# Kernel optimization log

Hardware: AMD Instinct MI355X
Metric: run time of the kernel (lower is better)

Reference implementation:

```python
import jax, jax.numpy as jnp
import numpy as np

N = 50000
E = 400000
C_IN = 32
H = 64
RATIO = 0.5
SEQ_LEN = 5


def setup_inputs() -> dict:
    key = jax.random.key(0)
    ks = jax.random.split(key, 12)
    x = jax.random.normal(ks[0], (N, C_IN), jnp.float32)
    row = jax.random.randint(ks[1], (E,), 0, N, jnp.int32)
    off = jax.random.randint(ks[2], (E,), 1, N, jnp.int32)
    col = ((row + off) % N).astype(jnp.int32)  # no self-loops
    edge_index = jnp.stack([row, col])
    mask = jax.random.uniform(ks[3], (N,)) < 0.5

    def g(k, shape, fan):
        return jax.random.normal(k, shape, jnp.float32) / np.float32(np.sqrt(fan))

    return {
        "x": x, "edge_index": edge_index, "mask": mask,
        "conv0_w": g(ks[4], (C_IN, H), C_IN), "conv0_b": jnp.zeros((H,), jnp.float32),
        "conv1_w": g(ks[5], (H, H), H), "conv1_b": jnp.zeros((H,), jnp.float32),
        "pool_w": g(ks[6], (H,), H),
        "up_w": g(ks[7], (H, H), H), "up_b": jnp.zeros((H,), jnp.float32),
        "lstm0_w_ih": g(ks[8], (4 * H, H), H), "lstm0_w_hh": g(ks[9], (4 * H, H), H),
        "lstm0_b_ih": jnp.zeros((4 * H,), jnp.float32), "lstm0_b_hh": jnp.zeros((4 * H,), jnp.float32),
        "fin_w_ih": g(ks[10], (4 * H, H), H), "fin_w_hh": g(ks[11], (4 * H, H), H),
        "fin_b_ih": jnp.zeros((4 * H,), jnp.float32), "fin_b_hh": jnp.zeros((4 * H,), jnp.float32),
    }


def _coalesce(row, col, w, n):
    # sum duplicate (row, col) entries; output sorted by (row, col)
    key = row.astype(np.int64) * n + col.astype(np.int64)
    uk, inv = np.unique(key, return_inverse=True)
    w2 = np.bincount(inv, weights=w.astype(np.float64), minlength=uk.shape[0]).astype(np.float32)
    return uk // n, uk % n, w2


def _augment_adj(row, col, w, n):
    # remove self loops, add self loops (weight 1), compute A @ A (sparse), remove self loops
    m = row != col
    row = np.concatenate([row[m].astype(np.int64), np.arange(n, dtype=np.int64)])
    col = np.concatenate([col[m].astype(np.int64), np.arange(n, dtype=np.int64)])
    w = np.concatenate([w[m].astype(np.float32), np.ones(n, np.float32)])
    row, col, w = _coalesce(row, col, w, n)  # CSR-ordered
    cnt = np.bincount(row, minlength=n)
    indptr = np.concatenate([[0], np.cumsum(cnt)])
    dk = cnt[col]                      # out-degree of middle node k for each edge (i,k)
    starts = indptr[col]
    total = int(dk.sum())
    seg = np.repeat(np.cumsum(dk) - dk, dk)
    gi = np.repeat(starts, dk) + (np.arange(total) - seg)
    oi = np.repeat(row, dk)
    oj = col[gi]
    ow = np.repeat(w, dk) * w[gi]
    r2, c2, w2 = _coalesce(oi, oj, ow, n)
    m2 = r2 != c2
    return r2[m2], c2[m2], w2[m2]


def _gcn(x, row, col, ew, n, W, b):
    # GCNConv(improved=True): self-loop weight 2.0, symmetric deg^-1/2 normalization,
    # aggregate messages at target (col)
    h = x @ W
    loop = jnp.arange(n, dtype=row.dtype)
    r = jnp.concatenate([row, loop])
    c = jnp.concatenate([col, loop])
    w = jnp.concatenate([ew, jnp.full((n,), 2.0, ew.dtype)])
    deg = jax.ops.segment_sum(w, c, num_segments=n)
    dinv = jnp.where(deg > 0, jax.lax.rsqrt(deg), 0.0)
    norm = dinv[r] * w * dinv[c]
    out = jax.ops.segment_sum(norm[:, None] * h[r], c, num_segments=n)
    return out + b


def _sequences(x, mi):
    # sliding window [idx-L+1, idx] per masked node, zero left-padded
    t = mi[:, None] + jnp.arange(SEQ_LEN)[None, :] - (SEQ_LEN - 1)  # [M, L]
    return jnp.where((t >= 0)[:, :, None], x[jnp.clip(t, 0)], 0.0)


def _lstm_last(seq, w_ih, w_hh, b_ih, b_hh):
    # torch LSTM gate order: i, f, g, o; zero init state; return last hidden
    h = jnp.zeros((seq.shape[0], w_hh.shape[1]), seq.dtype)
    c = jnp.zeros_like(h)
    def step(carry, xt):
        h, c = carry
        g = xt @ w_ih.T + h @ w_hh.T + b_ih + b_hh
        i, f, gg, o = jnp.split(g, 4, axis=-1)
        c = jax.nn.sigmoid(f) * c + jax.nn.sigmoid(i) * jnp.tanh(gg)
        h = jax.nn.sigmoid(o) * jnp.tanh(c)
        return (h, c), None
    (h, _), _ = jax.lax.scan(step, (h, c), jnp.swapaxes(seq, 0, 1))
    return h


def reference(x, edge_index, mask, conv0_w, conv0_b, conv1_w, conv1_b, pool_w,
              up_w, up_b, lstm0_w_ih, lstm0_w_hh, lstm0_b_ih, lstm0_b_hh,
              fin_w_ih, fin_w_hh, fin_b_ih, fin_b_hh):
    n = x.shape[0]
    row0, col0 = edge_index[0], edge_index[1]
    ew0 = jnp.ones((row0.shape[0],), x.dtype)

    # down conv 0
    x1 = jax.nn.relu(_gcn(x, row0, col0, ew0, n, conv0_w, conv0_b))

    # augment_adj: sparse (A+I)^2 without diagonal (structural, constant)
    r2, c2, w2 = _augment_adj(np.asarray(row0), np.asarray(col0),
                              np.ones(row0.shape[0], np.float32), n)

    # TopKPooling: score = tanh((x.w)/||w||), keep top ceil(ratio*n)
    score = jnp.tanh((x1 @ pool_w) / jnp.linalg.norm(pool_w))
    k = int(np.ceil(RATIO * n))
    perm = np.argsort(-np.asarray(score), kind="stable")[:k]
    remap = np.full(n, -1, np.int64)
    remap[perm] = np.arange(k)
    keep = (remap[r2] >= 0) & (remap[c2] >= 0)
    pr = jnp.asarray(remap[r2[keep]].astype(np.int32))
    pc = jnp.asarray(remap[c2[keep]].astype(np.int32))
    pw = jnp.asarray(w2[keep])
    permj = jnp.asarray(perm.astype(np.int32))
    xp = x1[permj] * score[permj][:, None]

    # down conv 1 on pooled graph
    x2 = jax.nn.relu(_gcn(xp, pr, pc, pw, k, conv1_w, conv1_b))

    # up path (depth=1): LSTM over skip features at masked nodes
    mi = jnp.asarray(np.where(np.asarray(mask))[0].astype(np.int32))
    h0 = _lstm_last(_sequences(x1, mi), lstm0_w_ih, lstm0_w_hh, lstm0_b_ih, lstm0_b_hh)
    res = x1.at[mi].set(h0)
    up = jnp.zeros_like(x1).at[permj].set(x2)
    xo = _gcn(res + up, row0, col0, ew0, n, up_w, up_b)  # last level: no activation

    # final LSTM on masked nodes
    hf = _lstm_last(_sequences(xo, mi), fin_w_ih, fin_w_hh, fin_b_ih, fin_b_hh)
    return xo.at[mi].set(hf)
```

## Files before the change

### kernel.cpp

```cpp
#include <hip/hip_runtime.h>
#include <math.h>

#define NN 50000
#define EE 400000
#define CINV 32
#define KKEEP 25000
#define SEQL 5
#define HASH_BITS 20
#define HASH_SIZE (1u<<HASH_BITS)
#define HASH_MASK (HASH_SIZE-1u)
#define HEMPTY 0xFFFFFFFFu
#define PSB 196

typedef float vf4 __attribute__((ext_vector_type(4)));

__device__ __forceinline__ float sigm(float x){ return __builtin_amdgcn_rcpf(1.f+__expf(-x)); }
__device__ __forceinline__ float ftanh(float x){ return 1.f - 2.f*__builtin_amdgcn_rcpf(1.f+__expf(2.f*x)); }

__global__ void k_init(uint2* __restrict__ hash, unsigned* __restrict__ hist,
                       int* __restrict__ degcnt, int* __restrict__ diagint,
                       int* __restrict__ fillc, int* __restrict__ minv,
                       unsigned* scal, unsigned long long* selp,
                       const float* __restrict__ w0, const float* __restrict__ b0i,
                       const float* __restrict__ b0h, const float* __restrict__ wf,
                       const float* __restrict__ bfi, const float* __restrict__ bfh,
                       float* __restrict__ WT0, float* __restrict__ WTf,
                       float* __restrict__ bs0, float* __restrict__ bsf){
  int i = blockIdx.x*256 + threadIdx.x;
  if (i < (int)HASH_SIZE) hash[i] = make_uint2(HEMPTY, 0u);
  if (i < 4*65536) hist[i] = 0u;
  if (i < NN){ degcnt[i]=0; diagint[i]=0; fillc[i]=0; minv[i]=-1; }
  if (i < 256*64){
    int g = i>>6, k = i&63;
    WT0[k*256+g] = w0[i];
    WTf[k*256+g] = wf[i];
  }
  if (i < 256){ bs0[i]=b0i[i]+b0h[i]; bsf[i]=bfi[i]+bfh[i]; }
  if (i == 0){ scal[0]=0u; scal[1]=0u; scal[3]=KKEEP; selp[0]=0ull; }
}

__global__ void k_phase2(const int* __restrict__ row, const int* __restrict__ col,
                         const int* __restrict__ mp, int* __restrict__ degcnt,
                         uint2* __restrict__ tab, unsigned* scal){
  int e = blockIdx.x*256 + threadIdx.x;
  if (e < EE){
    int c = col[e];
    atomicAdd(&degcnt[c], 1);
    unsigned key = (unsigned)row[e]*50000u + (unsigned)c;
    unsigned h = (key*2654435761u) >> (32-HASH_BITS);
    for(;;){
      unsigned old = atomicCAS(&tab[h].x, HEMPTY, key);
      if (old==HEMPTY || old==key){ atomicAdd(&tab[h].y, 1u); break; }
      h = (h+1)&HASH_MASK;
    }
  }
  if (e < NN/4){ if ((unsigned)mp[e] > 1u) atomicOr(&scal[1], 1u); }
}

__global__ void k_psum1(const int* __restrict__ deg, int* __restrict__ part,
                        int* __restrict__ bsum, float* __restrict__ dinv){
  __shared__ int sc[256];
  int b = blockIdx.x, t = threadIdx.x, i = b*256+t;
  int v = (i<NN) ? deg[i] : 0;
  if (i < NN) dinv[i] = rsqrtf((float)v + 2.0f);
  sc[t] = v; __syncthreads();
  for (int o=1;o<256;o<<=1){
    int x = (t>=o) ? sc[t-o] : 0;
    __syncthreads();
    sc[t] += x;
    __syncthreads();
  }
  if (i < NN) part[i] = sc[t]-v;
  if (t == 255) bsum[b] = sc[255];
}
__global__ void k_psum2(const int* __restrict__ bsum, int* __restrict__ boff){
  __shared__ int sc[256];
  int t = threadIdx.x;
  int v = (t<PSB) ? bsum[t] : 0;
  sc[t] = v; __syncthreads();
  for (int o=1;o<256;o<<=1){
    int x = (t>=o) ? sc[t-o] : 0;
    __syncthreads();
    sc[t] += x;
    __syncthreads();
  }
  if (t < PSB) boff[t] = sc[t]-v;
}
__global__ void k_psum3(const int* __restrict__ part, const int* __restrict__ boff,
                        int* __restrict__ indptr){
  int i = blockIdx.x*256 + threadIdx.x;
  if (i < NN) indptr[i] = part[i] + boff[blockIdx.x];
  if (i == 0) indptr[NN] = EE;
}

__global__ void k_phase4(const int* __restrict__ row, const int* __restrict__ col,
                         const int* __restrict__ indptr, int* __restrict__ fillc,
                         int* __restrict__ csr_r, const uint2* __restrict__ tab,
                         int* __restrict__ diagint, const void* __restrict__ mp,
                         unsigned* scal, int* __restrict__ mlist, int* __restrict__ minv){
  int idx = blockIdx.x*256 + threadIdx.x;
  if (idx < EE){
    int r = row[idx], c = col[idx];
    int pos = indptr[c] + atomicAdd(&fillc[c], 1);
    csr_r[pos] = r;
    unsigned rkey = (unsigned)c*50000u + (unsigned)r;
    unsigned h = (rkey*2654435761u) >> (32-HASH_BITS);
    for(;;){
      unsigned kk = tab[h].x;
      if (kk==rkey){ atomicAdd(&diagint[r], (int)tab[h].y); break; }
      if (kk==HEMPTY) break;
      h = (h+1)&HASH_MASK;
    }
  } else {
    int i = idx - EE;
    if (i < NN){
      int mv = scal[1] ? (int)((const unsigned char*)mp)[i] : ((const int*)mp)[i];
      if (mv){ int p = (int)atomicAdd(&scal[0], 1u); mlist[p] = i; minv[i] = p; }
    }
  }
}

__global__ void k_mm_h0v(const float* __restrict__ X, const float* __restrict__ W, float* __restrict__ Y){
  int idx = blockIdx.x*256 + threadIdx.x;
  if (idx >= NN*16) return;
  int i = idx>>4, fq = idx&15;
  const vf4* X4 = (const vf4*)&X[i*CINV];
  const vf4* W4 = (const vf4*)W;
  vf4 acc = {0.f,0.f,0.f,0.f};
  #pragma unroll
  for (int kq=0;kq<CINV/4;kq++){
    vf4 xv = X4[kq];
    #pragma unroll
    for (int u=0;u<4;u++) acc += xv[u] * W4[(kq*4+u)*16+fq];
  }
  ((vf4*)Y)[i*16+fq] = acc;
}
__global__ void k_mm64v(const float* __restrict__ X, const float* __restrict__ W, float* __restrict__ Y){
  int idx = blockIdx.x*256 + threadIdx.x;
  if (idx >= NN*16) return;
  int i = idx>>4, fq = idx&15;
  const vf4* X4 = (const vf4*)&X[i*64];
  const vf4* W4 = (const vf4*)W;
  vf4 acc = {0.f,0.f,0.f,0.f};
  #pragma unroll
  for (int kq=0;kq<16;kq++){
    vf4 xv = X4[kq];
    #pragma unroll
    for (int u=0;u<4;u++) acc += xv[u] * W4[(kq*4+u)*16+fq];
  }
  ((vf4*)Y)[i*16+fq] = acc;
}
__global__ void k_mm64sv(const float* __restrict__ X, const float* __restrict__ W,
                         const float* __restrict__ sc, const int* __restrict__ kp,
                         float* __restrict__ Y){
  int idx = blockIdx.x*256 + threadIdx.x;
  if (idx >= NN*16) return;
  int i = idx>>4, fq = idx&15;
  if (!kp[i]) return;
  const vf4* X4 = (const vf4*)&X[i*64];
  const vf4* W4 = (const vf4*)W;
  vf4 acc = {0.f,0.f,0.f,0.f};
  #pragma unroll
  for (int kq=0;kq<16;kq++){
    vf4 xv = X4[kq];
    #pragma unroll
    for (int u=0;u<4;u++) acc += xv[u] * W4[(kq*4+u)*16+fq];
  }
  float s = sc[i];
  acc *= s;
  ((vf4*)Y)[i*16+fq] = acc;
}

__global__ void g_gcn0(const int* __restrict__ indptr, const int* __restrict__ csr_r,
                       const float* __restrict__ dinv, const float* __restrict__ H,
                       const float* __restrict__ b, const float* __restrict__ pw,
                       float* __restrict__ out, unsigned long long* __restrict__ keys,
                       float* __restrict__ score, unsigned* __restrict__ hist){
  int node = blockIdx.x*4 + (threadIdx.x>>6), lane = threadIdx.x&63;
  if (node >= NN) return;
  int s = __builtin_amdgcn_readfirstlane(indptr[node]);
  int e = __builtin_amdgcn_readfirstlane(indptr[node+1]);
  int deg = e - s;
  float a0=0.f,a1=0.f,a2=0.f,a3=0.f;
  for (int base=0; base<deg; base+=64){
    int take = min(64, deg-base);
    bool act = lane < take;
    int ii = act ? csr_r[s+base+lane] : 0;
    float dv = act ? dinv[ii] : 0.f;
    int j=0;
    for (; j+4<=take; j+=4){
      int r0=__shfl(ii,j,64), r1=__shfl(ii,j+1,64), r2=__shfl(ii,j+2,64), r3=__shfl(ii,j+3,64);
      float d0=__shfl(dv,j,64), d1=__shfl(dv,j+1,64), d2=__shfl(dv,j+2,64), d3=__shfl(dv,j+3,64);
      a0 += d0*H[(size_t)r0*64+lane];
      a1 += d1*H[(size_t)r1*64+lane];
      a2 += d2*H[(size_t)r2*64+lane];
      a3 += d3*H[(size_t)r3*64+lane];
    }
    for (; j<take; j++){
      int r0=__shfl(ii,j,64); float d0=__shfl(dv,j,64);
      a0 += d0*H[(size_t)r0*64+lane];
    }
  }
  float acc = (a0+a1)+(a2+a3);
  float di = dinv[node];
  float v = di*acc + 2.f*di*di*H[(size_t)node*64+lane] + b[lane];
  float x1v = fmaxf(v, 0.f);
  out[(size_t)node*64+lane] = x1v;
  float pv = pw[lane];
  float nq = pv*pv;
  float dq = x1v*pv;
  for (int o=32;o;o>>=1){ nq += __shfl_down(nq, o, 64); dq += __shfl_down(dq, o, 64); }
  if (lane==0){
    float sv = tanhf(dq / sqrtf(nq));
    sv = sv + 0.0f;
    score[node] = sv;
    unsigned u = __float_as_uint(sv);
    unsigned asc = (u>>31) ? ~u : (u | 0x80000000u);
    unsigned desc = ~asc;
    keys[node] = (((unsigned long long)desc)<<32) | (unsigned)node;
    atomicAdd(&hist[desc>>16], 1u);
  }
}
__global__ void g_t2(const int* __restrict__ indptr, const int* __restrict__ csr_r,
                     const float* __restrict__ dinv1, const float* __restrict__ hp,
                     float* __restrict__ t2){
  int node = blockIdx.x*4 + (threadIdx.x>>6), lane = threadIdx.x&63;
  if (node >= NN) return;
  int s = __builtin_amdgcn_readfirstlane(indptr[node]);
  int e = __builtin_amdgcn_readfirstlane(indptr[node+1]);
  int deg = e - s;
  float a0 = dinv1[node]*hp[(size_t)node*64+lane];
  float a1 = 0.f;
  for (int base=0; base<deg; base+=64){
    int take = min(64, deg-base);
    bool act = lane < take;
    int ii = act ? csr_r[s+base+lane] : 0;
    float dv = act ? dinv1[ii] : 0.f;
    int j=0;
    for (; j+2<=take; j+=2){
      float d0=__shfl(dv,j,64), d1=__shfl(dv,j+1,64);
      int r0=__shfl(ii,j,64), r1=__shfl(ii,j+1,64);
      if (d0!=0.f) a0 += d0*hp[(size_t)r0*64+lane];
      if (d1!=0.f) a1 += d1*hp[(size_t)r1*64+lane];
    }
    for (; j<take; j++){
      float d0=__shfl(dv,j,64); int r0=__shfl(ii,j,64);
      if (d0!=0.f) a0 += d0*hp[(size_t)r0*64+lane];
    }
  }
  t2[(size_t)node*64+lane] = a0+a1;
}
__global__ void g_agg2y(const int* __restrict__ indptr, const int* __restrict__ csr_r,
                        const float* __restrict__ t2, const float* __restrict__ hp,
                        const float* __restrict__ dinv1, const int* __restrict__ diagint,
                        const int* __restrict__ kp, const float* __restrict__ b1,
                        const float* __restrict__ C, const float* __restrict__ Hbuf,
                        const int* __restrict__ minv, float* __restrict__ D){
  int node = blockIdx.x*4 + (threadIdx.x>>6), lane = threadIdx.x&63;
  if (node >= NN) return;
  int mv = minv[node];
  float base = (mv >= 0) ? Hbuf[(size_t)mv*64+lane] : C[(size_t)node*64+lane];
  float add = 0.f;
  if (kp[node]){
    int s = __builtin_amdgcn_readfirstlane(indptr[node]);
    int e = __builtin_amdgcn_readfirstlane(indptr[node+1]);
    int deg = e - s;
    float a0 = t2[(size_t)node*64+lane];
    float a1=0.f,a2=0.f,a3=0.f;
    for (int bs2=0; bs2<deg; bs2+=64){
      int take = min(64, deg-bs2);
      bool act = lane < take;
      int ii = act ? csr_r[s+bs2+lane] : 0;
      int j=0;
      for (; j+4<=take; j+=4){
        int r0=__shfl(ii,j,64), r1=__shfl(ii,j+1,64), r2=__shfl(ii,j+2,64), r3=__shfl(ii,j+3,64);
        a0 += t2[(size_t)r0*64+lane];
        a1 += t2[(size_t)r1*64+lane];
        a2 += t2[(size_t)r2*64+lane];
        a3 += t2[(size_t)r3*64+lane];
      }
      for (; j<take; j++){
        int r0=__shfl(ii,j,64);
        a0 += t2[(size_t)r0*64+lane];
      }
    }
    float acc = (a0+a1)+(a2+a3);
    float di = dinv1[node], hv = hp[(size_t)node*64+lane];
    float diag = (float)(diagint[node] + 1);
    float v = di*(acc - diag*di*hv) + 2.f*di*di*hv + b1[lane];
    add = fmaxf(v, 0.f);
  }
  D[(size_t)node*64+lane] = base + add;
}
__global__ void g_up(const int* __restrict__ indptr, const int* __restrict__ csr_r,
                     const float* __restrict__ dinv, const float* __restrict__ H,
                     const float* __restrict__ b, float* __restrict__ xo, float* __restrict__ out){
  int node = blockIdx.x*4 + (threadIdx.x>>6), lane = threadIdx.x&63;
  if (node >= NN) return;
  int s = __builtin_amdgcn_readfirstlane(indptr[node]);
  int e = __builtin_amdgcn_readfirstlane(indptr[node+1]);
  int deg = e - s;
  float a0=0.f,a1=0.f,a2=0.f,a3=0.f;
  for (int base=0; base<deg; base+=64){
    int take = min(64, deg-base);
    bool act = lane < take;
    int ii = act ? csr_r[s+base+lane] : 0;
    float dv = act ? dinv[ii] : 0.f;
    int j=0;
    for (; j+4<=take; j+=4){
      int r0=__shfl(ii,j,64), r1=__shfl(ii,j+1,64), r2=__shfl(ii,j+2,64), r3=__shfl(ii,j+3,64);
      float d0=__shfl(dv,j,64), d1=__shfl(dv,j+1,64), d2=__shfl(dv,j+2,64), d3=__shfl(dv,j+3,64);
      a0 += d0*H[(size_t)r0*64+lane];
      a1 += d1*H[(size_t)r1*64+lane];
      a2 += d2*H[(size_t)r2*64+lane];
      a3 += d3*H[(size_t)r3*64+lane];
    }
    for (; j<take; j++){
      int r0=__shfl(ii,j,64); float d0=__shfl(dv,j,64);
      a0 += d0*H[(size_t)r0*64+lane];
    }
  }
  float acc = (a0+a1)+(a2+a3);
  float di = dinv[node];
  float v = di*acc + 2.f*di*di*H[(size_t)node*64+lane] + b[lane];
  xo[(size_t)node*64+lane] = v; out[(size_t)node*64+lane] = v;
}

__global__ void k_hist(const unsigned long long* __restrict__ keys, unsigned* __restrict__ hist,
                       const unsigned long long* __restrict__ selp, int round){
  int i = blockIdx.x*256 + threadIdx.x;
  if (i >= NN) return;
  unsigned long long key = keys[i];
  int shift = 48 - 16*round;
  if ((key>>(shift+16)) == selp[0])
    atomicAdd(&hist[(unsigned)((key>>shift)&0xFFFFull)], 1u);
}
__global__ void k_pick(const unsigned* __restrict__ hist, unsigned long long* selp, unsigned* scal){
  __shared__ unsigned csum[256];
  __shared__ unsigned bins[256];
  __shared__ int schunk;
  int t = threadIdx.x;
  const uint4* h4 = (const uint4*)(hist + t*256);
  unsigned s = 0;
  #pragma unroll 8
  for (int j=0;j<64;j++){ uint4 v = h4[j]; s += v.x+v.y+v.z+v.w; }
  csum[t] = s;
  __syncthreads();
  if (t==0){
    unsigned rem = scal[3];
    int chunk = 255;
    for (int c2=0;c2<256;c2++){ unsigned cc=csum[c2]; if (rem>cc) rem-=cc; else { chunk=c2; break; } }
    schunk = chunk; scal[3] = rem;
  }
  __syncthreads();
  bins[t] = hist[schunk*256 + t];
  __syncthreads();
  if (t==0){
    unsigned rem = scal[3];
    int bin = schunk*256 + 255;
    for (int b=0;b<256;b++){ unsigned hv=bins[b]; if (rem>hv) rem-=hv; else { bin = schunk*256 + b; break; } }
    selp[0] = (selp[0]<<16) | (unsigned long long)(unsigned)bin;
    scal[3] = rem;
  }
}
__global__ void k_tsg(const int* __restrict__ indptr, const int* __restrict__ csr_r,
                      const unsigned long long* __restrict__ keys,
                      const unsigned long long* __restrict__ selp,
                      int* __restrict__ kp, int* __restrict__ ts){
  int i = blockIdx.x*256 + threadIdx.x;
  if (i >= NN) return;
  unsigned long long sp = selp[0];
  int s = indptr[i], e = indptr[i+1];
  int self = (keys[i] <= sp) ? 1 : 0;
  kp[i] = self;
  int acc = self;
  for (int j=s;j<e;j++) acc += (keys[csr_r[j]] <= sp) ? 1 : 0;
  ts[i] = acc;
}
__global__ void k_csg(const int* __restrict__ indptr, const int* __restrict__ csr_r,
                      const int* __restrict__ ts, const int* __restrict__ diagint,
                      const int* __restrict__ kp, float* __restrict__ dinv1){
  int i = blockIdx.x*256 + threadIdx.x;
  if (i >= NN) return;
  int s = indptr[i], e = indptr[i+1];
  int acc = ts[i];
  for (int j=s;j<e;j++) acc += ts[csr_r[j]];
  dinv1[i] = kp[i] ? rsqrtf((float)(acc - diagint[i] - 1) + 2.0f) : 0.f;
}

__global__ __launch_bounds__(256) void k_xw(const float* __restrict__ src,
        const float* __restrict__ WT, const float* __restrict__ bsum,
        float* __restrict__ XW){
  __shared__ vf4 Wl[4096];
  int t = threadIdx.x;
  const vf4* Wg = (const vf4*)WT;
  for (int u=t; u<4096; u+=256) Wl[u] = Wg[u];
  int fq = t & 63, wv = t >> 6;
  vf4 bias = ((const vf4*)bsum)[fq];
  __syncthreads();
  for (int g = blockIdx.x*4 + wv; g < NN/4; g += gridDim.x*4){
    int n0 = g*4;
    const vf4* X4 = (const vf4*)&src[(size_t)n0*64];
    vf4 a0=bias, a1=bias, a2=bias, a3=bias;
    #pragma unroll 4
    for (int kq=0;kq<16;kq++){
      vf4 x0 = X4[kq], x1 = X4[16+kq], x2 = X4[32+kq], x3 = X4[48+kq];
      vf4 w0 = Wl[(kq*4+0)*64+fq];
      vf4 w1 = Wl[(kq*4+1)*64+fq];
      vf4 w2 = Wl[(kq*4+2)*64+fq];
      vf4 w3 = Wl[(kq*4+3)*64+fq];
      a0 += x0.x*w0 + x0.y*w1 + x0.z*w2 + x0.w*w3;
      a1 += x1.x*w0 + x1.y*w1 + x1.z*w2 + x1.w*w3;
      a2 += x2.x*w0 + x2.y*w1 + x2.z*w2 + x2.w*w3;
      a3 += x3.x*w0 + x3.y*w1 + x3.z*w2 + x3.w*w3;
    }
    vf4* Y = (vf4*)XW;
    Y[(size_t)n0*64 + fq]       = a0;
    Y[(size_t)n0*64 + 64 + fq]  = a1;
    Y[(size_t)n0*64 + 128 + fq] = a2;
    Y[(size_t)n0*64 + 192 + fq] = a3;
  }
}

__global__ __launch_bounds__(256) void k_rec(const float* __restrict__ XW,
        const float* __restrict__ whh, const float* __restrict__ bsum,
        const int* __restrict__ mlist, const unsigned* __restrict__ scal,
        float* __restrict__ dst, int scatter){
  int M = (int)scal[0];
  if (M < 0 || M > NN) M = 0;
  int w = threadIdx.x>>6, lane = threadIdx.x&63;
  int r = w*64 + lane;
  const vf4* g4 = (const vf4*)&whh[(size_t)r*64];
  vf4 wh[16];
  #pragma unroll
  for (int j=0;j<16;j++) wh[j] = g4[j];
  __shared__ float sh[8][64];
  __shared__ float gates[8][4][64];
  int ntask = (M+7)>>3;
  for (int task = blockIdx.x; task < ntask; task += gridDim.x){
    int m0 = task*8 + 2*w, m1 = m0+1;
    bool v0 = (m0 < M), v1 = (m1 < M);
    int n0 = mlist[v0 ? m0 : (M-1)];
    int n1 = mlist[v1 ? m1 : (M-1)];
    n0 = min(max(n0, 0), NN-1);
    n1 = min(max(n1, 0), NN-1);
    float c0, h0, c1, h1;
    float x0,x1,x2,x3, y0,y1,y2,y3;
    {
      int ra = n0 - (SEQL-1), rb = n1 - (SEQL-1);
      if (ra >= 0){
        const float* p = &XW[(size_t)ra*256];
        x0=p[lane]; x1=p[64+lane]; x2=p[128+lane]; x3=p[192+lane];
      } else { x0=bsum[lane]; x1=bsum[64+lane]; x2=bsum[128+lane]; x3=bsum[192+lane]; }
      if (rb >= 0){
        const float* p = &XW[(size_t)rb*256];
        y0=p[lane]; y1=p[64+lane]; y2=p[128+lane]; y3=p[192+lane];
      } else { y0=bsum[lane]; y1=bsum[64+lane]; y2=bsum[128+lane]; y3=bsum[192+lane]; }
      c0 = sigm(x0)*ftanh(x2); h0 = sigm(x3)*ftanh(c0);
      c1 = sigm(y0)*ftanh(y2); h1 = sigm(y3)*ftanh(c1);
      sh[2*w][lane] = h0;
      sh[2*w+1][lane] = h1;
    }
    __syncthreads();
    for (int t=1;t<SEQL;t++){
      int ra = n0 - (SEQL-1) + t, rb = n1 - (SEQL-1) + t;
      if (ra >= 0){
        const float* p = &XW[(size_t)ra*256];
        x0=p[lane]; x1=p[64+lane]; x2=p[128+lane]; x3=p[192+lane];
      } else { x0=bsum[lane]; x1=bsum[64+lane]; x2=bsum[128+lane]; x3=bsum[192+lane]; }
      if (rb >= 0){
        const float* p = &XW[(size_t)rb*256];
        y0=p[lane]; y1=p[64+lane]; y2=p[128+lane]; y3=p[192+lane];
      } else { y0=bsum[lane]; y1=bsum[64+lane]; y2=bsum[128+lane]; y3=bsum[192+lane]; }
      vf4 a0={0,0,0,0},a1={0,0,0,0},a2={0,0,0,0},a3={0,0,0,0};
      vf4 a4={0,0,0,0},a5={0,0,0,0},a6={0,0,0,0},a7={0,0,0,0};
      #pragma unroll
      for (int j=0;j<16;j++){
        vf4 wj = wh[j];
        a0 += (*(const vf4*)&sh[0][j*4]) * wj;
        a1 += (*(const vf4*)&sh[1][j*4]) * wj;
        a2 += (*(const vf4*)&sh[2][j*4]) * wj;
        a3 += (*(const vf4*)&sh[3][j*4]) * wj;
        a4 += (*(const vf4*)&sh[4][j*4]) * wj;
        a5 += (*(const vf4*)&sh[5][j*4]) * wj;
        a6 += (*(const vf4*)&sh[6][j*4]) * wj;
        a7 += (*(const vf4*)&sh[7][j*4]) * wj;
      }
      gates[0][w][lane] = a0.x+a0.y+a0.z+a0.w;
      gates[1][w][lane] = a1.x+a1.y+a1.z+a1.w;
      gates[2][w][lane] = a2.x+a2.y+a2.z+a2.w;
      gates[3][w][lane] = a3.x+a3.y+a3.z+a3.w;
      gates[4][w][lane] = a4.x+a4.y+a4.z+a4.w;
      gates[5][w][lane] = a5.x+a5.y+a5.z+a5.w;
      gates[6][w][lane] = a6.x+a6.y+a6.z+a6.w;
      gates[7][w][lane] = a7.x+a7.y+a7.z+a7.w;
      __syncthreads();
      int p0 = 2*w, p1 = 2*w+1;
      float gi = gates[p0][0][lane] + x0;
      float gf = gates[p0][1][lane] + x1;
      float gg = gates[p0][2][lane] + x2;
      float go = gates[p0][3][lane] + x3;
      c0 = sigm(gf)*c0 + sigm(gi)*ftanh(gg);
      h0 = sigm(go)*ftanh(c0);
      sh[p0][lane] = h0;
      gi = gates[p1][0][lane] + y0;
      gf = gates[p1][1][lane] + y1;
      gg = gates[p1][2][lane] + y2;
      go = gates[p1][3][lane] + y3;
      c1 = sigm(gf)*c1 + sigm(gi)*ftanh(gg);
      h1 = sigm(go)*ftanh(c1);
      sh[p1][lane] = h1;
      __syncthreads();
    }
    if (v0){
      size_t o = scatter ? ((size_t)n0*64 + lane) : ((size_t)m0*64 + lane);
      dst[o] = h0;
    }
    if (v1){
      size_t o = scatter ? ((size_t)n1*64 + lane) : ((size_t)m1*64 + lane);
      dst[o] = h1;
    }
  }
}

extern "C" void kernel_launch(void* const* d_in, const int* in_sizes, int n_in,
                              void* d_out, int out_size, void* d_ws, size_t ws_size,
                              hipStream_t stream) {
  const float* x   = (const float*)d_in[0];
  const int*   ei  = (const int*)d_in[1];
  const int*   row = ei;
  const int*   col = ei + EE;
  const void*  mp  = d_in[2];
  const float* W0  = (const float*)d_in[3];
  const float* b0  = (const float*)d_in[4];
  const float* W1  = (const float*)d_in[5];
  const float* b1  = (const float*)d_in[6];
  const float* pw  = (const float*)d_in[7];
  const float* Wu  = (const float*)d_in[8];
  const float* bu  = (const float*)d_in[9];
  const float* l0wih=(const float*)d_in[10];
  const float* l0whh=(const float*)d_in[11];
  const float* l0bih=(const float*)d_in[12];
  const float* l0bhh=(const float*)d_in[13];
  const float* lfwih=(const float*)d_in[14];
  const float* lfwhh=(const float*)d_in[15];
  const float* lfbih=(const float*)d_in[16];
  const float* lfbhh=(const float*)d_in[17];

  char* wp = (char*)d_ws;
  auto alloc = [&](size_t bytes)->char*{ char* p = wp; wp += ((bytes+255)/256)*256; return p; };
  float* A     = (float*)alloc((size_t)NN*64*4);
  float* B     = (float*)alloc((size_t)NN*64*4);
  float* C     = (float*)alloc((size_t)NN*64*4);
  float* D     = (float*)alloc((size_t)NN*64*4);
  float* Ebuf  = (float*)alloc((size_t)NN*64*4);
  float* Hbuf  = (float*)alloc((size_t)NN*64*4);
  float* XW    = (float*)alloc((size_t)NN*256*4);
  float* WT0   = (float*)alloc((size_t)256*64*4);
  float* WTf   = (float*)alloc((size_t)256*64*4);
  float* bs0   = (float*)alloc((size_t)256*4);
  float* bsf   = (float*)alloc((size_t)256*4);
  float* score = (float*)alloc((size_t)NN*4);
  float* dinv0 = (float*)alloc((size_t)NN*4);
  float* dinv1 = (float*)alloc((size_t)NN*4);
  unsigned long long* keys = (unsigned long long*)alloc((size_t)NN*8);
  int* degcnt  = (int*)alloc((size_t)NN*4);
  int* diagint = (int*)alloc((size_t)NN*4);
  int* ts      = (int*)alloc((size_t)NN*4);
  int* kp      = (int*)alloc((size_t)NN*4);
  int* mlist   = (int*)alloc((size_t)NN*4);
  int* minv    = (int*)alloc((size_t)NN*4);
  int* indptr  = (int*)alloc((size_t)(NN+1)*4);
  int* part    = (int*)alloc((size_t)NN*4);
  int* fillc   = (int*)alloc((size_t)NN*4);
  int* bsum    = (int*)alloc((size_t)256*4);
  int* boff    = (int*)alloc((size_t)256*4);
  int* csr_r   = (int*)alloc((size_t)EE*4);
  uint2* hash  = (uint2*)alloc((size_t)HASH_SIZE*8);
  unsigned* hist=(unsigned*)alloc((size_t)4*65536*4);
  unsigned* scal=(unsigned*)alloc(256);
  unsigned long long* selp = (unsigned long long*)(scal + 4);

  #define GRID1(n) dim3(((n)+255)/256), dim3(256), 0, stream
  #define GRIDW dim3((NN+3)/4), dim3(256), 0, stream

  k_init<<<GRID1(HASH_SIZE)>>>(hash, hist, degcnt, diagint, fillc, minv,
                               scal, selp, l0wih, l0bih, l0bhh, lfwih, lfbih, lfbhh,
                               WT0, WTf, bs0, bsf);
  k_phase2<<<GRID1(EE)>>>(row, col, (const int*)mp, degcnt, hash, scal);
  k_psum1<<<dim3(PSB),dim3(256),0,stream>>>(degcnt, part, bsum, dinv0);
  k_psum2<<<dim3(1),dim3(256),0,stream>>>(bsum, boff);
  k_psum3<<<dim3(PSB),dim3(256),0,stream>>>(part, boff, indptr);
  k_phase4<<<GRID1(EE+NN)>>>(row, col, indptr, fillc, csr_r, hash, diagint, mp, scal, mlist, minv);

  k_mm_h0v<<<GRID1(NN*16)>>>(x, W0, A);
  g_gcn0<<<GRIDW>>>(indptr, csr_r, dinv0, A, b0, pw, C, keys, score, hist);

  k_pick<<<dim3(1),dim3(256),0,stream>>>(hist, selp, scal);
  for (int r2=1;r2<4;r2++){
    k_hist<<<GRID1(NN)>>>(keys, hist + r2*65536, selp, r2);
    k_pick<<<dim3(1),dim3(256),0,stream>>>(hist + r2*65536, selp, scal);
  }
  k_tsg<<<GRID1(NN)>>>(indptr, csr_r, keys, selp, kp, ts);
  k_csg<<<GRID1(NN)>>>(indptr, csr_r, ts, diagint, kp, dinv1);

  k_mm64sv<<<GRID1(NN*16)>>>(C, W1, score, kp, Ebuf);
  g_t2<<<GRIDW>>>(indptr, csr_r, dinv1, Ebuf, A);

  k_xw<<<dim3(512),dim3(256),0,stream>>>(C, WT0, bs0, XW);
  k_rec<<<dim3(2048),dim3(256),0,stream>>>(XW, l0whh, bs0, mlist, scal, Hbuf, 0);

  g_agg2y<<<GRIDW>>>(indptr, csr_r, A, Ebuf, dinv1, diagint, kp, b1, C, Hbuf, minv, D);

  k_mm64v<<<GRID1(NN*16)>>>(D, Wu, Ebuf);
  g_up<<<GRIDW>>>(indptr, csr_r, dinv0, Ebuf, bu, B, (float*)d_out);

  k_xw<<<dim3(512),dim3(256),0,stream>>>(B, WTf, bsf, XW);
  k_rec<<<dim3(2048),dim3(256),0,stream>>>(XW, lfwhh, bsf, mlist, scal, (float*)d_out, 1);
  #undef GRIDW
  #undef GRID1
}
```

Before: 688.7 us.

## Fuse small kernels to cut launches and shrink LSTM tasks to one sequence per wave

Folds the first dense matmul into the edge hashing kernel and the pooled matmul into the degree-count kernel. It also merges the two prefix-sum passes so each block rescans the block sums itself, which removes three launches from a launch-bound pipeline. The LSTM recurrence kernel now handles one sequence per wave (four per block) instead of two, with fewer blocks launched. This cuts per-wave register and shared-memory work but halves the sequences sharing each loaded recurrent weight set.

```diff
diff --git a/kernel.cpp b/kernel.cpp
--- a/kernel.cpp
+++ b/kernel.cpp
@@ -41,12 +41,14 @@
 
 __global__ void k_phase2(const int* __restrict__ row, const int* __restrict__ col,
                          const int* __restrict__ mp, int* __restrict__ degcnt,
-                         uint2* __restrict__ tab, unsigned* scal){
-  int e = blockIdx.x*256 + threadIdx.x;
-  if (e < EE){
-    int c = col[e];
+                         uint2* __restrict__ tab, unsigned* scal,
+                         const float* __restrict__ X, const float* __restrict__ W,
+                         float* __restrict__ Y){
+  int idx = blockIdx.x*256 + threadIdx.x;
+  if (idx < EE){
+    int c = col[idx];
     atomicAdd(&degcnt[c], 1);
-    unsigned key = (unsigned)row[e]*50000u + (unsigned)c;
+    unsigned key = (unsigned)row[idx]*50000u + (unsigned)c;
     unsigned h = (key*2654435761u) >> (32-HASH_BITS);
     for(;;){
       unsigned old = atomicCAS(&tab[h].x, HEMPTY, key);
@@ -54,7 +56,20 @@
       h = (h+1)&HASH_MASK;
     }
   }
-  if (e < NN/4){ if ((unsigned)mp[e] > 1u) atomicOr(&scal[1], 1u); }
+  if (idx < NN/4){ if ((unsigned)mp[idx] > 1u) atomicOr(&scal[1], 1u); }
+  if (idx < NN*16){
+    int i = idx>>4, fq = idx&15;
+    const vf4* X4 = (const vf4*)&X[i*CINV];
+    const vf4* W4 = (const vf4*)W;
+    vf4 acc = {0.f,0.f,0.f,0.f};
+    #pragma unroll
+    for (int kq=0;kq<CINV/4;kq++){
+      vf4 xv = X4[kq];
+      #pragma unroll
+      for (int u=0;u<4;u++) acc += xv[u] * W4[(kq*4+u)*16+fq];
+    }
+    ((vf4*)Y)[i*16+fq] = acc;
+  }
 }
 
 __global__ void k_psum1(const int* __restrict__ deg, int* __restrict__ part,
@@ -73,7 +88,8 @@
   if (i < NN) part[i] = sc[t]-v;
   if (t == 255) bsum[b] = sc[255];
 }
-__global__ void k_psum2(const int* __restrict__ bsum, int* __restrict__ boff){
+__global__ void k_psum3(const int* __restrict__ part, const int* __restrict__ bsum,
+                        int* __restrict__ indptr){
   __shared__ int sc[256];
   int t = threadIdx.x;
   int v = (t<PSB) ? bsum[t] : 0;
@@ -84,12 +100,10 @@
     sc[t] += x;
     __syncthreads();
   }
-  if (t < PSB) boff[t] = sc[t]-v;
-}
-__global__ void k_psum3(const int* __restrict__ part, const int* __restrict__ boff,
-                        int* __restrict__ indptr){
-  int i = blockIdx.x*256 + threadIdx.x;
-  if (i < NN) indptr[i] = part[i] + boff[blockIdx.x];
+  int bb = blockIdx.x;
+  int ex = sc[bb] - ((bb<PSB) ? bsum[bb] : 0);
+  int i = bb*256 + t;
+  if (i < NN) indptr[i] = part[i] + ex;
   if (i == 0) indptr[NN] = EE;
 }
 
@@ -120,21 +134,6 @@
   }
 }
 
-__global__ void k_mm_h0v(const float* __restrict__ X, const float* __restrict__ W, float* __restrict__ Y){
-  int idx = blockIdx.x*256 + threadIdx.x;
-  if (idx >= NN*16) return;
-  int i = idx>>4, fq = idx&15;
-  const vf4* X4 = (const vf4*)&X[i*CINV];
-  const vf4* W4 = (const vf4*)W;
-  vf4 acc = {0.f,0.f,0.f,0.f};
-  #pragma unroll
-  for (int kq=0;kq<CINV/4;kq++){
-    vf4 xv = X4[kq];
-    #pragma unroll
-    for (int u=0;u<4;u++) acc += xv[u] * W4[(kq*4+u)*16+fq];
-  }
-  ((vf4*)Y)[i*16+fq] = acc;
-}
 __global__ void k_mm64v(const float* __restrict__ X, const float* __restrict__ W, float* __restrict__ Y){
   int idx = blockIdx.x*256 + threadIdx.x;
   if (idx >= NN*16) return;
@@ -148,26 +147,6 @@
     #pragma unroll
     for (int u=0;u<4;u++) acc += xv[u] * W4[(kq*4+u)*16+fq];
   }
-  ((vf4*)Y)[i*16+fq] = acc;
-}
-__global__ void k_mm64sv(const float* __restrict__ X, const float* __restrict__ W,
-                         const float* __restrict__ sc, const int* __restrict__ kp,
-                         float* __restrict__ Y){
-  int idx = blockIdx.x*256 + threadIdx.x;
-  if (idx >= NN*16) return;
-  int i = idx>>4, fq = idx&15;
-  if (!kp[i]) return;
-  const vf4* X4 = (const vf4*)&X[i*64];
-  const vf4* W4 = (const vf4*)W;
-  vf4 acc = {0.f,0.f,0.f,0.f};
-  #pragma unroll
-  for (int kq=0;kq<16;kq++){
-    vf4 xv = X4[kq];
-    #pragma unroll
-    for (int u=0;u<4;u++) acc += xv[u] * W4[(kq*4+u)*16+fq];
-  }
-  float s = sc[i];
-  acc *= s;
   ((vf4*)Y)[i*16+fq] = acc;
 }
 
@@ -377,15 +356,34 @@
   for (int j=s;j<e;j++) acc += (keys[csr_r[j]] <= sp) ? 1 : 0;
   ts[i] = acc;
 }
-__global__ void k_csg(const int* __restrict__ indptr, const int* __restrict__ csr_r,
-                      const int* __restrict__ ts, const int* __restrict__ diagint,
-                      const int* __restrict__ kp, float* __restrict__ dinv1){
-  int i = blockIdx.x*256 + threadIdx.x;
-  if (i >= NN) return;
-  int s = indptr[i], e = indptr[i+1];
-  int acc = ts[i];
-  for (int j=s;j<e;j++) acc += ts[csr_r[j]];
-  dinv1[i] = kp[i] ? rsqrtf((float)(acc - diagint[i] - 1) + 2.0f) : 0.f;
+__global__ void k_csgmm(const int* __restrict__ indptr, const int* __restrict__ csr_r,
+                        const int* __restrict__ ts, const int* __restrict__ diagint,
+                        const int* __restrict__ kp, float* __restrict__ dinv1,
+                        const float* __restrict__ X, const float* __restrict__ W,
+                        const float* __restrict__ sc, float* __restrict__ Y){
+  int idx = blockIdx.x*256 + threadIdx.x;
+  if (idx < NN*16){
+    int i = idx>>4, fq = idx&15;
+    if (!kp[i]) return;
+    const vf4* X4 = (const vf4*)&X[i*64];
+    const vf4* W4 = (const vf4*)W;
+    vf4 acc = {0.f,0.f,0.f,0.f};
+    #pragma unroll
+    for (int kq=0;kq<16;kq++){
+      vf4 xv = X4[kq];
+      #pragma unroll
+      for (int u=0;u<4;u++) acc += xv[u] * W4[(kq*4+u)*16+fq];
+    }
+    acc *= sc[i];
+    ((vf4*)Y)[i*16+fq] = acc;
+  } else {
+    int i = idx - NN*16;
+    if (i >= NN) return;
+    int s = indptr[i], e = indptr[i+1];
+    int acc = ts[i];
+    for (int j=s;j<e;j++) acc += ts[csr_r[j]];
+    dinv1[i] = kp[i] ? rsqrtf((float)(acc - diagint[i] - 1) + 2.0f) : 0.f;
+  }
 }
 
 __global__ __launch_bounds__(256) void k_xw(const float* __restrict__ src,
@@ -434,46 +432,38 @@
   vf4 wh[16];
   #pragma unroll
   for (int j=0;j<16;j++) wh[j] = g4[j];
-  __shared__ float sh[8][64];
-  __shared__ float gates[8][4][64];
-  int ntask = (M+7)>>3;
+  __shared__ float sh[4][64];
+  __shared__ float gates[4][4][64];
+  int ntask = (M+3)>>2;
   for (int task = blockIdx.x; task < ntask; task += gridDim.x){
-    int m0 = task*8 + 2*w, m1 = m0+1;
-    bool v0 = (m0 < M), v1 = (m1 < M);
-    int n0 = mlist[v0 ? m0 : (M-1)];
-    int n1 = mlist[v1 ? m1 : (M-1)];
-    n0 = min(max(n0, 0), NN-1);
-    n1 = min(max(n1, 0), NN-1);
-    float c0, h0, c1, h1;
-    float x0,x1,x2,x3, y0,y1,y2,y3;
+    int m = task*4 + w;
+    bool valid = (m < M);
+    int node = mlist[valid ? m : (M-1)];
+    node = min(max(node, 0), NN-1);
+    float c, h;
+    float x0,x1,x2,x3;
     {
-      int ra = n0 - (SEQL-1), rb = n1 - (SEQL-1);
-      if (ra >= 0){
-        const float* p = &XW[(size_t)ra*256];
+      int rowi = node - (SEQL-1);
+      if (rowi >= 0){
+        const float* p = &XW[(size_t)rowi*256];
         x0=p[lane]; x1=p[64+lane]; x2=p[128+lane]; x3=p[192+lane];
-      } else { x0=bsum[lane]; x1=bsum[64+lane]; x2=bsum[128+lane]; x3=bsum[192+lane]; }
-      if (rb >= 0){
-        const float* p = &XW[(size_t)rb*256];
-        y0=p[lane]; y1=p[64+lane]; y2=p[128+lane]; y3=p[192+lane];
-      } else { y0=bsum[lane]; y1=bsum[64+lane]; y2=bsum[128+lane]; y3=bsum[192+lane]; }
-      c0 = sigm(x0)*ftanh(x2); h0 = sigm(x3)*ftanh(c0);
-      c1 = sigm(y0)*ftanh(y2); h1 = sigm(y3)*ftanh(c1);
-      sh[2*w][lane] = h0;
-      sh[2*w+1][lane] = h1;
+      } else {
+        x0=bsum[lane]; x1=bsum[64+lane]; x2=bsum[128+lane]; x3=bsum[192+lane];
+      }
+      c = sigm(x0)*ftanh(x2);
+      h = sigm(x3)*ftanh(c);
+      sh[w][lane] = h;
     }
     __syncthreads();
     for (int t=1;t<SEQL;t++){
-      int ra = n0 - (SEQL-1) + t, rb = n1 - (SEQL-1) + t;
-      if (ra >= 0){
-        const float* p = &XW[(size_t)ra*256];
+      int rowi = node - (SEQL-1) + t;
+      if (rowi >= 0){
+        const float* p = &XW[(size_t)rowi*256];
         x0=p[lane]; x1=p[64+lane]; x2=p[128+lane]; x3=p[192+lane];
-      } else { x0=bsum[lane]; x1=bsum[64+lane]; x2=bsum[128+lane]; x3=bsum[192+lane]; }
-      if (rb >= 0){
-        const float* p = &XW[(size_t)rb*256];
-        y0=p[lane]; y1=p[64+lane]; y2=p[128+lane]; y3=p[192+lane];
-      } else { y0=bsum[lane]; y1=bsum[64+lane]; y2=bsum[128+lane]; y3=bsum[192+lane]; }
-      vf4 a0={0,0,0,0},a1={0,0,0,0},a2={0,0,0,0},a3={0,0,0,0};
-      vf4 a4={0,0,0,0},a5={0,0,0,0},a6={0,0,0,0},a7={0,0,0,0};
+      } else {
+        x0=bsum[lane]; x1=bsum[64+lane]; x2=bsum[128+lane]; x3=bsum[192+lane];
+      }
+      vf4 a0={0,0,0,0}, a1={0,0,0,0}, a2={0,0,0,0}, a3={0,0,0,0};
       #pragma unroll
       for (int j=0;j<16;j++){
         vf4 wj = wh[j];
@@ -481,44 +471,24 @@
         a1 += (*(const vf4*)&sh[1][j*4]) * wj;
         a2 += (*(const vf4*)&sh[2][j*4]) * wj;
         a3 += (*(const vf4*)&sh[3][j*4]) * wj;
-        a4 += (*(const vf4*)&sh[4][j*4]) * wj;
-        a5 += (*(const vf4*)&sh[5][j*4]) * wj;
-        a6 += (*(const vf4*)&sh[6][j*4]) * wj;
-        a7 += (*(const vf4*)&sh[7][j*4]) * wj;
       }
       gates[0][w][lane] = a0.x+a0.y+a0.z+a0.w;
       gates[1][w][lane] = a1.x+a1.y+a1.z+a1.w;
       gates[2][w][lane] = a2.x+a2.y+a2.z+a2.w;
       gates[3][w][lane] = a3.x+a3.y+a3.z+a3.w;
-      gates[4][w][lane] = a4.x+a4.y+a4.z+a4.w;
-      gates[5][w][lane] = a5.x+a5.y+a5.z+a5.w;
-      gates[6][w][lane] = a6.x+a6.y+a6.z+a6.w;
-      gates[7][w][lane] = a7.x+a7.y+a7.z+a7.w;
       __syncthreads();
-      int p0 = 2*w, p1 = 2*w+1;
-      float gi = gates[p0][0][lane] + x0;
-      float gf = gates[p0][1][lane] + x1;
-      float gg = gates[p0][2][lane] + x2;
-      float go = gates[p0][3][lane] + x3;
-      c0 = sigm(gf)*c0 + sigm(gi)*ftanh(gg);
-      h0 = sigm(go)*ftanh(c0);
-      sh[p0][lane] = h0;
-      gi = gates[p1][0][lane] + y0;
-      gf = gates[p1][1][lane] + y1;
-      gg = gates[p1][2][lane] + y2;
-      go = gates[p1][3][lane] + y3;
-      c1 = sigm(gf)*c1 + sigm(gi)*ftanh(gg);
-      h1 = sigm(go)*ftanh(c1);
-      sh[p1][lane] = h1;
+      float gi = gates[w][0][lane] + x0;
+      float gf = gates[w][1][lane] + x1;
+      float gg = gates[w][2][lane] + x2;
+      float go = gates[w][3][lane] + x3;
+      c = sigm(gf)*c + sigm(gi)*ftanh(gg);
+      h = sigm(go)*ftanh(c);
+      sh[w][lane] = h;
       __syncthreads();
     }
-    if (v0){
-      size_t o = scatter ? ((size_t)n0*64 + lane) : ((size_t)m0*64 + lane);
-      dst[o] = h0;
-    }
-    if (v1){
-      size_t o = scatter ? ((size_t)n1*64 + lane) : ((size_t)m1*64 + lane);
-      dst[o] = h1;
+    if (valid){
+      size_t o = scatter ? ((size_t)node*64 + lane) : ((size_t)m*64 + lane);
+      dst[o] = h;
     }
   }
 }
@@ -574,7 +544,6 @@
   int* part    = (int*)alloc((size_t)NN*4);
   int* fillc   = (int*)alloc((size_t)NN*4);
   int* bsum    = (int*)alloc((size_t)256*4);
-  int* boff    = (int*)alloc((size_t)256*4);
   int* csr_r   = (int*)alloc((size_t)EE*4);
   uint2* hash  = (uint2*)alloc((size_t)HASH_SIZE*8);
   unsigned* hist=(unsigned*)alloc((size_t)4*65536*4);
@@ -587,13 +556,11 @@
   k_init<<<GRID1(HASH_SIZE)>>>(hash, hist, degcnt, diagint, fillc, minv,
                                scal, selp, l0wih, l0bih, l0bhh, lfwih, lfbih, lfbhh,
                                WT0, WTf, bs0, bsf);
-  k_phase2<<<GRID1(EE)>>>(row, col, (const int*)mp, degcnt, hash, scal);
+  k_phase2<<<GRID1(NN*16)>>>(row, col, (const int*)mp, degcnt, hash, scal, x, W0, A);
   k_psum1<<<dim3(PSB),dim3(256),0,stream>>>(degcnt, part, bsum, dinv0);
-  k_psum2<<<dim3(1),dim3(256),0,stream>>>(bsum, boff);
-  k_psum3<<<dim3(PSB),dim3(256),0,stream>>>(part, boff, indptr);
+  k_psum3<<<dim3(PSB),dim3(256),0,stream>>>(part, bsum, indptr);
   k_phase4<<<GRID1(EE+NN)>>>(row, col, indptr, fillc, csr_r, hash, diagint, mp, scal, mlist, minv);
 
-  k_mm_h0v<<<GRID1(NN*16)>>>(x, W0, A);
   g_gcn0<<<GRIDW>>>(indptr, csr_r, dinv0, A, b0, pw, C, keys, score, hist);
 
   k_pick<<<dim3(1),dim3(256),0,stream>>>(hist, selp, scal);
@@ -602,13 +569,11 @@
     k_pick<<<dim3(1),dim3(256),0,stream>>>(hist + r2*65536, selp, scal);
   }
   k_tsg<<<GRID1(NN)>>>(indptr, csr_r, keys, selp, kp, ts);
-  k_csg<<<GRID1(NN)>>>(indptr, csr_r, ts, diagint, kp, dinv1);
-
-  k_mm64sv<<<GRID1(NN*16)>>>(C, W1, score, kp, Ebuf);
+  k_csgmm<<<GRID1(NN*16+NN)>>>(indptr, csr_r, ts, diagint, kp, dinv1, C, W1, score, Ebuf);
   g_t2<<<GRIDW>>>(indptr, csr_r, dinv1, Ebuf, A);
 
   k_xw<<<dim3(512),dim3(256),0,stream>>>(C, WT0, bs0, XW);
-  k_rec<<<dim3(2048),dim3(256),0,stream>>>(XW, l0whh, bs0, mlist, scal, Hbuf, 0);
+  k_rec<<<dim3(1024),dim3(256),0,stream>>>(XW, l0whh, bs0, mlist, scal, Hbuf, 0);
 
   g_agg2y<<<GRIDW>>>(indptr, csr_r, A, Ebuf, dinv1, diagint, kp, b1, C, Hbuf, minv, D);
 
@@ -616,7 +581,7 @@
   g_up<<<GRIDW>>>(indptr, csr_r, dinv0, Ebuf, bu, B, (float*)d_out);
 
   k_xw<<<dim3(512),dim3(256),0,stream>>>(B, WTf, bsf, XW);
-  k_rec<<<dim3(2048),dim3(256),0,stream>>>(XW, lfwhh, bsf, mlist, scal, (float*)d_out, 1);
+  k_rec<<<dim3(1024),dim3(256),0,stream>>>(XW, lfwhh, bsf, mlist, scal, (float*)d_out, 1);
   #undef GRIDW
   #undef GRID1
 }
```

Result: faster. 661.0 us (-4.0%).
